# Kernel optimization log

Hardware: AMD Instinct MI355X
Metric: run time of the kernel (lower is better)

The kernel has to match this reference:

```python
import jax, jax.numpy as jnp
import numpy as np

B, C, H, W = 8, 256, 64, 64
K = 64  # tfam_channels

def _conv3x3(x, w, b):
    # x: [B,C,H,W], w: [O,I,3,3]
    y = jax.lax.conv_general_dilated(x, w, window_strides=(1, 1), padding='SAME',
                                     dimension_numbers=('NCHW', 'OIHW', 'NCHW'))
    return y + b[None, :, None, None]

def setup_inputs() -> dict:
    key = jax.random.key(0)
    ks = jax.random.split(key, 5)
    s1 = 1.0 / np.sqrt(C)
    s3 = 1.0 / np.sqrt(C * 9)
    return {
        'x': jax.random.normal(ks[0], (B, C, H, W), jnp.float32),
        'top_w': jax.random.normal(ks[1], (K, C), jnp.float32) * s1,
        'top_b': jnp.zeros((K,), jnp.float32),
        'center_w': jax.random.normal(ks[2], (K, C), jnp.float32) * s1,
        'center_b': jnp.zeros((K,), jnp.float32),
        'bottom_w': jax.random.normal(ks[3], (C, C, 3, 3), jnp.float32) * s3,
        'bottom_b': jnp.zeros((C,), jnp.float32),
        'out_w': jax.random.normal(ks[4], (C, C, 3, 3), jnp.float32) * s3,
        'out_b': jnp.zeros((C,), jnp.float32),
    }

def reference(x, top_w, top_b, center_w, center_b, bottom_w, bottom_b, out_w, out_b):
    b, c, h, w = x.shape
    hw = h * w
    # 1x1 convs as channel contractions
    x_top = jnp.einsum('bchw,kc->bkhw', x, top_w) + top_b[None, :, None, None]
    x_center = jnp.einsum('bchw,kc->bkhw', x, center_w) + center_b[None, :, None, None]
    x_bottom = _conv3x3(x, bottom_w, bottom_b)

    x_top = x_top.reshape(b, -1, hw)                     # [B,K,HW]
    x_center = x_center.reshape(b, -1, hw)               # [B,K,HW]
    x_bot = x_bottom.reshape(b, c, hw).transpose(0, 2, 1)  # [B,HW,C]

    sp_map = jnp.einsum('bkn,bkm->bnm', x_center, x_top)  # [B,HW,HW]
    # global softmax over the entire flattened map per batch element
    sp_map = jax.nn.softmax(sp_map.reshape(b, -1), axis=1).reshape(b, hw, hw)
    sp_map = jnp.einsum('bnm,bmc->bnc', sp_map, x_bot)    # [B,HW,C]
    # faithful raw reshape (as in the torch code: no transpose)
    sp_map = sp_map.reshape(b, c, h, w)
    y = x + sp_map
    return _conv3x3(y, out_w, out_b)
```

## Files before the change

kernel.cpp:

```cpp
#include <hip/hip_runtime.h>

using bf16x8 = __attribute__((ext_vector_type(8))) short;
using f16x8  = __attribute__((ext_vector_type(8))) _Float16;
using f32x4  = __attribute__((ext_vector_type(4))) float;

#define DEVI static __device__ __forceinline__

DEVI unsigned short f2bf(float f){
  unsigned u = __builtin_bit_cast(unsigned, f);
  u += 0x7fffu + ((u >> 16) & 1u);
  return (unsigned short)(u >> 16);
}
DEVI float bf2f(unsigned short h){
  unsigned u = ((unsigned)h) << 16;
  return __builtin_bit_cast(float, u);
}
DEVI unsigned short f2h(float f){
  _Float16 h = (_Float16)f;
  return __builtin_bit_cast(unsigned short, h);
}
DEVI f32x4 zf4(){ f32x4 z; z[0]=0.f; z[1]=0.f; z[2]=0.f; z[3]=0.f; return z; }
DEVI unsigned cvtpk(float lo, float hi){
  unsigned r;
  asm("v_cvt_pk_bf16_f32 %0, %1, %2" : "=v"(r) : "v"(lo), "v"(hi));
  return r;
}

__global__ __launch_bounds__(256) void k_prep(
    const float* __restrict__ top_w, const float* __restrict__ cen_w,
    const float* __restrict__ bot_w, const float* __restrict__ out_w,
    float* __restrict__ wTt, float* __restrict__ wTc,
    unsigned short* __restrict__ apb, unsigned short* __restrict__ apo){
  int i = blockIdx.x * 256 + threadIdx.x;
  if (i < 64 * 256){
    int c = i >> 6, k = i & 63;
    wTt[i] = top_w[k * 256 + c];
    wTc[i] = cen_w[k * 256 + c];
  }
  if (i < 9 * 256 * 256){
    int tau = i >> 16, oc = i & 65535;
    apb[i] = f2bf(bot_w[oc * 9 + tau]);
    apo[i] = f2bf(out_w[oc * 9 + tau]);
  }
}

__global__ __launch_bounds__(256) void k_topcenter(
    const float* __restrict__ x,
    const float* __restrict__ wTt, const float* __restrict__ wTc,
    const float* __restrict__ top_b, const float* __restrict__ cen_b,
    unsigned short* __restrict__ tT16, unsigned short* __restrict__ cT16){
  __shared__ float xs[16][256];
  int bid = blockIdx.x;
  int b = bid & 7, z = (bid >> 3) & 1, nt = (bid >> 4) & 15, kq = bid >> 8;
  int t = threadIdx.x;
  int n = nt * 256 + t;
  int k0 = kq * 16;
  const float* wT   = z ? wTc : wTt;
  const float* bias = z ? cen_b : top_b;
  unsigned short* o16 = z ? cT16 : tT16;
  const float scale = z ? 1.0f : 1.4426950408889634f;
  const float* xb = x + ((size_t)b << 20);

  float acc[16];
  #pragma unroll
  for (int k = 0; k < 16; k++) acc[k] = 0.f;

  for (int cc = 0; cc < 256; cc += 16){
    __syncthreads();
    #pragma unroll
    for (int r = 0; r < 16; r++)
      xs[r][t] = xb[((size_t)(cc + r) << 12) + nt * 256 + t];
    __syncthreads();
    #pragma unroll
    for (int r = 0; r < 16; r++){
      float xv = xs[r][t];
      const float* wr = wT + (cc + r) * 64 + k0;
      #pragma unroll
      for (int k = 0; k < 16; k++) acc[k] = fmaf(wr[k], xv, acc[k]);
    }
  }
  size_t base = (((size_t)b << 12) + n) * 64 + k0;
  #pragma unroll
  for (int k8 = 0; k8 < 16; k8 += 8){
    bf16x8 v8;
    #pragma unroll
    for (int j = 0; j < 8; j++)
      v8[j] = (short)f2h((acc[k8 + j] + bias[k0 + k8 + j]) * scale);
    *(bf16x8*)(o16 + base + k8) = v8;
  }
}

__global__ __launch_bounds__(256) void k_transx(
    const float* __restrict__ x, unsigned short* __restrict__ ocl){
  __shared__ float tile[32][33];
  int b = blockIdx.z, ct = blockIdx.y, pt = blockIdx.x;
  int tx = threadIdx.x & 31, ty = threadIdx.x >> 5;
  size_t bo = (size_t)b << 20;
  int c0 = ct * 32, p0 = pt * 32;
  #pragma unroll
  for (int q = 0; q < 4; q++){
    int c = c0 + ty + q * 8;
    tile[ty + q * 8][tx] = x[bo + ((size_t)c << 12) + p0 + tx];
  }
  __syncthreads();
  #pragma unroll
  for (int q = 0; q < 4; q++){
    int p = p0 + ty + q * 8;
    ocl[bo + ((size_t)p << 8) + c0 + tx] = f2bf(tile[tx][ty + q * 8]);
  }
}

__global__ __launch_bounds__(256) void k_transy(
    const float* __restrict__ x, const unsigned short* __restrict__ U0,
    const unsigned short* __restrict__ U1, const float* __restrict__ Z,
    unsigned short* __restrict__ ocl){
  __shared__ float tile[32][33];
  int b = blockIdx.z, ct = blockIdx.y, pt = blockIdx.x;
  int tx = threadIdx.x & 31, ty = threadIdx.x >> 5;
  size_t bo = (size_t)b << 20;
  int c0 = ct * 32, p0 = pt * 32;
  float invZ = 1.0f / Z[b];
  #pragma unroll
  for (int q = 0; q < 4; q++){
    int c = c0 + ty + q * 8;
    size_t idx = bo + ((size_t)c << 12) + p0 + tx;
    float u = bf2f(U0[idx]);
    if (U1) u += bf2f(U1[idx]);
    tile[ty + q * 8][tx] = fmaf(u, invZ, x[idx]);
  }
  __syncthreads();
  #pragma unroll
  for (int q = 0; q < 4; q++){
    int p = p0 + ty + q * 8;
    ocl[bo + ((size_t)p << 8) + c0 + tx] = f2bf(tile[tx][ty + q * 8]);
  }
}

template<int OUTF32>
__global__ __launch_bounds__(256, 4) void k_conv3(
    const unsigned short* __restrict__ incl,
    const unsigned short* __restrict__ ap,
    const float* __restrict__ bias, void* __restrict__ outp){
  __shared__ unsigned short Xs[3][64][72];
  int bid = blockIdx.x;
  int b = bid & 7, h = (bid >> 3) & 63, oh = bid >> 9;
  int t = threadIdx.x, wv = t >> 6, l = t & 63, lr = l & 15, g = l >> 4;
  int o0 = oh * 128 + wv * 32;
  const unsigned short* inb = incl + ((size_t)b << 20);

  f32x4 acc[2][4];
  #pragma unroll
  for (int a = 0; a < 2; a++)
    #pragma unroll
    for (int c = 0; c < 4; c++) acc[a][c] = zf4();

  int sw = t >> 2, sco = (t & 3) * 16;
  const bf16x8 zero8 = {0,0,0,0,0,0,0,0};

  bf16x8 st[3][2];
  #pragma unroll
  for (int r = 0; r < 3; r++){
    int h2 = h + r - 1;
    bool v = (unsigned)h2 < 64u;
    #pragma unroll
    for (int u = 0; u < 2; u++)
      st[r][u] = v ? *(const bf16x8*)(inb + (((size_t)(h2 * 64 + sw)) << 8)
                                      + sco + u * 8)
                   : zero8;
  }

  for (int cc = 0; cc < 256; cc += 64){
    __syncthreads();
    #pragma unroll
    for (int r = 0; r < 3; r++)
      #pragma unroll
      for (int u = 0; u < 2; u++)
        *(bf16x8*)(&Xs[r][sw][sco + u * 8]) = st[r][u];
    __syncthreads();
    if (cc < 192){
      #pragma unroll
      for (int r = 0; r < 3; r++){
        int h2 = h + r - 1;
        bool v = (unsigned)h2 < 64u;
        #pragma unroll
        for (int u = 0; u < 2; u++)
          st[r][u] = v ? *(const bf16x8*)(inb + (((size_t)(h2 * 64 + sw)) << 8)
                                          + cc + 64 + sco + u * 8)
                       : zero8;
      }
    }
    #pragma unroll
    for (int tau = 0; tau < 9; tau++){
      int dy = tau / 3 - 1, dx = tau % 3 - 1;
      #pragma unroll
      for (int kf = 0; kf < 2; kf++){
        bf16x8 af[2];
        #pragma unroll
        for (int of = 0; of < 2; of++)
          af[of] = *(const bf16x8*)(ap + ((size_t)tau << 16)
                     + ((o0 + of * 16 + lr) << 8) + cc + kf * 32 + 8 * g);
        bf16x8 bv[4];
        #pragma unroll
        for (int pf = 0; pf < 4; pf++){
          int wsrc = pf * 16 + lr + dx;
          bv[pf] = ((unsigned)wsrc < 64u)
                 ? *(const bf16x8*)(&Xs[dy + 1][wsrc][kf * 32 + 8 * g])
                 : zero8;
        }
        #pragma unroll
        for (int of = 0; of < 2; of++)
          #pragma unroll
          for (int pf = 0; pf < 4; pf++){
            if (OUTF32)
              acc[of][pf] = __builtin_amdgcn_mfma_f32_16x16x32_bf16(af[of], bv[pf], acc[of][pf], 0, 0, 0);
            else
              acc[of][pf] = __builtin_amdgcn_mfma_f32_16x16x32_bf16(bv[pf], af[of], acc[of][pf], 0, 0, 0);
          }
      }
    }
  }
  if (OUTF32){
    #pragma unroll
    for (int of = 0; of < 2; of++){
      int ob = o0 + of * 16 + 4 * g;
      #pragma unroll
      for (int pf = 0; pf < 4; pf++){
        int p = h * 64 + pf * 16 + lr;
        #pragma unroll
        for (int i = 0; i < 4; i++){
          int o = ob + i;
          ((float*)outp)[((size_t)b << 20) + ((size_t)o << 12) + p]
              = acc[of][pf][i] + bias[o];
        }
      }
    }
  } else {
    unsigned short* xbt = (unsigned short*)outp;
    #pragma unroll
    for (int of = 0; of < 2; of++){
      int o = o0 + of * 16 + lr;
      float bo_ = bias[o];
      #pragma unroll
      for (int pf = 0; pf < 4; pf++){
        int mc = h * 8 + pf * 2 + (g >> 1);
        unsigned lo = cvtpk(acc[of][pf][0] + bo_, acc[of][pf][1] + bo_);
        unsigned hi = cvtpk(acc[of][pf][2] + bo_, acc[of][pf][3] + bo_);
        unsigned* dst = (unsigned*)(xbt
            + ((((size_t)b * 512 + mc) * 256 + o) * 8 + 4 * (g & 1)));
        dst[0] = lo;
        dst[1] = hi;
      }
    }
  }
}

__global__ __launch_bounds__(256, 2) void k_pv(
    const unsigned short* __restrict__ tT16, const unsigned short* __restrict__ cT16,
    const unsigned short* __restrict__ xbt,
    unsigned short* __restrict__ U0, unsigned short* __restrict__ U1,
    float* __restrict__ rsum, int nsteps){
  __shared__ unsigned short Xl[2][4][256][8];
  __shared__ unsigned short Pl[2][4][128][8];
  int bid = blockIdx.x;
  int b = bid & 7, nt = (bid >> 3) & 31, mh = bid >> 8;
  int t = threadIdx.x, wv = t >> 6, l = t & 63, lr = l & 15, g = l >> 4;
  int n0 = nt * 128;
  unsigned short* Ub = mh ? U1 : U0;

  f16x8 ch[2][4];
  #pragma unroll
  for (int kf = 0; kf < 2; kf++)
    #pragma unroll
    for (int nf = 0; nf < 4; nf++)
      ch[kf][nf] = *(const f16x8*)(cT16
          + (((size_t)b << 12) + n0 + (wv >> 1) * 64 + nf * 16 + lr) * 64
          + kf * 32 + 8 * g);

  f32x4 acc[8][4];
  #pragma unroll
  for (int a = 0; a < 8; a++)
    #pragma unroll
    for (int c = 0; c < 4; c++) acc[a][c] = zf4();
  float racc = 0.f;

  const unsigned short* tb = tT16
      + (((size_t)b << 12) + (size_t)mh * 2048 + (wv & 1) * 16 + lr) * 64 + 8 * g;

  const unsigned short* gsrc = xbt
      + (((size_t)b * 512 + (size_t)mh * 256) * 256 + wv * 64 + l) * 8;

  int mt2 = (wv & 1) * 2 + (g >> 1);
  f16x8 a0 = *(const f16x8*)(tb);
  f16x8 a1 = *(const f16x8*)(tb + 32);

  {
    #pragma unroll
    for (int j = 0; j < 4; j++)
      __builtin_amdgcn_global_load_lds(
          (const __attribute__((address_space(1))) void*)(gsrc + (size_t)j * 2048),
          (__attribute__((address_space(3))) void*)(&Xl[0][j][wv * 64][0]),
          16, 0, 0);
    f32x4 sa[4];
    #pragma unroll
    for (int nf = 0; nf < 4; nf++) sa[nf] = zf4();
    #pragma unroll
    for (int nf = 0; nf < 4; nf++)
      sa[nf] = __builtin_amdgcn_mfma_f32_16x16x32_f16(a0, ch[0][nf], sa[nf], 0, 0, 0);
    #pragma unroll
    for (int nf = 0; nf < 4; nf++)
      sa[nf] = __builtin_amdgcn_mfma_f32_16x16x32_f16(a1, ch[1][nf], sa[nf], 0, 0, 0);
    a0 = *(const f16x8*)(tb + 2048);
    a1 = *(const f16x8*)(tb + 2048 + 32);
    #pragma unroll
    for (int nf = 0; nf < 4; nf++){
      float e0 = __builtin_amdgcn_exp2f(sa[nf][0]);
      float e1 = __builtin_amdgcn_exp2f(sa[nf][1]);
      float e2 = __builtin_amdgcn_exp2f(sa[nf][2]);
      float e3 = __builtin_amdgcn_exp2f(sa[nf][3]);
      racc += (e0 + e1) + (e2 + e3);
      int n = (wv >> 1) * 64 + nf * 16 + lr;
      unsigned* pp = (unsigned*)(&Pl[0][mt2][n][(g & 1) * 4]);
      pp[0] = cvtpk(e0, e1);
      pp[1] = cvtpk(e2, e3);
    }
    __syncthreads();
  }

  for (int ms = 0; ms < nsteps; ms++){
    int cur = ms & 1, nxt = cur ^ 1;
    bool more = (ms + 1 < nsteps);
    f32x4 sa[4];
    #pragma unroll
    for (int nf = 0; nf < 4; nf++) sa[nf] = zf4();
    if (more){
      #pragma unroll
      for (int j = 0; j < 4; j++)
        __builtin_amdgcn_global_load_lds(
            (const __attribute__((address_space(1))) void*)(gsrc + (size_t)((ms + 1) * 4 + j) * 2048),
            (__attribute__((address_space(3))) void*)(&Xl[nxt][j][wv * 64][0]),
            16, 0, 0);
      #pragma unroll
      for (int nf = 0; nf < 4; nf++)
        sa[nf] = __builtin_amdgcn_mfma_f32_16x16x32_f16(a0, ch[0][nf], sa[nf], 0, 0, 0);
      #pragma unroll
      for (int nf = 0; nf < 4; nf++)
        sa[nf] = __builtin_amdgcn_mfma_f32_16x16x32_f16(a1, ch[1][nf], sa[nf], 0, 0, 0);
      if (ms + 2 < nsteps){
        a0 = *(const f16x8*)(tb + (size_t)(ms + 2) * 2048);
        a1 = *(const f16x8*)(tb + (size_t)(ms + 2) * 2048 + 32);
      }
    }
    {
      bf16x8 pa[8];
      #pragma unroll
      for (int nf = 0; nf < 8; nf++)
        pa[nf] = *(const bf16x8*)(&Pl[cur][g][nf * 16 + lr][0]);
      #pragma unroll
      for (int cf = 0; cf < 4; cf++){
        bf16x8 bx = *(const bf16x8*)(&Xl[cur][g][wv * 64 + cf * 16 + lr][0]);
        #pragma unroll
        for (int nf = 0; nf < 8; nf++)
          acc[nf][cf] = __builtin_amdgcn_mfma_f32_16x16x32_bf16(pa[nf], bx, acc[nf][cf], 0, 0, 0);
      }
    }
    if (more){
      #pragma unroll
      for (int nf = 0; nf < 4; nf++){
        float e0 = __builtin_amdgcn_exp2f(sa[nf][0]);
        float e1 = __builtin_amdgcn_exp2f(sa[nf][1]);
        float e2 = __builtin_amdgcn_exp2f(sa[nf][2]);
        float e3 = __builtin_amdgcn_exp2f(sa[nf][3]);
        racc += (e0 + e1) + (e2 + e3);
        int n = (wv >> 1) * 64 + nf * 16 + lr;
        unsigned* pp = (unsigned*)(&Pl[nxt][mt2][n][(g & 1) * 4]);
        pp[0] = cvtpk(e0, e1);
        pp[1] = cvtpk(e2, e3);
      }
    }
    __syncthreads();
  }

  #pragma unroll
  for (int nf = 0; nf < 8; nf++)
    #pragma unroll
    for (int cf = 0; cf < 4; cf++)
      #pragma unroll
      for (int i = 0; i < 4; i++){
        int n = n0 + nf * 16 + 4 * g + i;
        int c = wv * 64 + cf * 16 + lr;
        __builtin_nontemporal_store(f2bf(acc[nf][cf][i]),
            &Ub[((size_t)b << 20) + ((size_t)n << 8) + c]);
      }
  racc += __shfl_xor(racc, 1);
  racc += __shfl_xor(racc, 2);
  racc += __shfl_xor(racc, 4);
  racc += __shfl_xor(racc, 8);
  racc += __shfl_xor(racc, 16);
  racc += __shfl_xor(racc, 32);
  if (l == 0) rsum[(size_t)bid * 4 + wv] = racc;
}

__global__ __launch_bounds__(256) void k_rsum(const float* __restrict__ r,
                                              float* __restrict__ Z, int total){
  __shared__ float red[256];
  int b = blockIdx.x, t = threadIdx.x;
  float s = 0.f;
  for (int s2 = t; s2 < total; s2 += 256)
    s += r[(size_t)(b + 8 * (s2 >> 2)) * 4 + (s2 & 3)];
  red[t] = s;
  __syncthreads();
  for (int o = 128; o > 0; o >>= 1){
    if (t < o) red[t] += red[t + o];
    __syncthreads();
  }
  if (t == 0) Z[b] = red[0];
}

extern "C" void kernel_launch(void* const* d_in, const int* in_sizes, int n_in,
                              void* d_out, int out_size, void* d_ws, size_t ws_size,
                              hipStream_t stream) {
  const float* x     = (const float*)d_in[0];
  const float* top_w = (const float*)d_in[1];
  const float* top_b = (const float*)d_in[2];
  const float* cen_w = (const float*)d_in[3];
  const float* cen_b = (const float*)d_in[4];
  const float* bot_w = (const float*)d_in[5];
  const float* bot_b = (const float*)d_in[6];
  const float* out_w = (const float*)d_in[7];
  const float* out_b = (const float*)d_in[8];
  float* out = (float*)d_out;

  constexpr size_t MB = 1ull << 20;
  int msplit = (ws_size >= 80 * MB) ? 2 : 1;

  char* p = (char*)d_ws;
  unsigned short* U0 = (unsigned short*)p;     p += 16 * MB;
  unsigned short* U1 = nullptr;
  if (msplit == 2){ U1 = (unsigned short*)p;   p += 16 * MB; }
  unsigned short* tT16 = (unsigned short*)p;   p += 4 * MB;
  unsigned short* cT16 = (unsigned short*)p;   p += 4 * MB;
  unsigned short* xbt  = (unsigned short*)p;   p += 16 * MB;
  unsigned short* xcl  = (unsigned short*)p;   p += 16 * MB;
  float* wTt = (float*)p;                      p += 65536;
  float* wTc = (float*)p;                      p += 65536;
  unsigned short* apb = (unsigned short*)p;    p += 1179648;
  unsigned short* apo = (unsigned short*)p;    p += 1179648;
  float* r = (float*)p;                        p += 65536;
  float* Z = (float*)p;

  int grid_pv = 8 * 32 * msplit;
  int nsteps  = (4096 / msplit) / 32;
  int slots   = (grid_pv / 8) * 4;

  k_prep<<<2304, 256, 0, stream>>>(top_w, cen_w, bot_w, out_w, wTt, wTc, apb, apo);
  k_topcenter<<<dim3(1024), 256, 0, stream>>>(x, wTt, wTc, top_b, cen_b,
                                              tT16, cT16);
  k_transx<<<dim3(128, 8, 8), 256, 0, stream>>>(x, xcl);
  k_conv3<0><<<dim3(1024), 256, 0, stream>>>(xcl, apb, bot_b, (void*)xbt);
  k_pv<<<dim3(grid_pv), 256, 0, stream>>>(tT16, cT16, xbt, U0,
                                          msplit == 2 ? U1 : U0, r, nsteps);
  k_rsum<<<8, 256, 0, stream>>>(r, Z, slots);
  k_transy<<<dim3(128, 8, 8), 256, 0, stream>>>(x, U0, U1, Z, xcl);
  k_conv3<1><<<dim3(1024), 256, 0, stream>>>(xcl, apo, out_b, (void*)out);
}
```

Measured before the change: 304.4 us.

## Split PV reduction four ways over M and hand-schedule barriers in k_pv

Raises the split of the attention's M (key) dimension from two to four when the workspace is large enough. This quadruples the k_pv grid for better CU occupancy, and k_transy now sums four bf16 partial buffers. It also replaces __syncthreads with explicit lgkmcnt waits, s_barrier and sched_barrier fences, and drops the barrier after the final step, to cut redundant waits. The cost is extra partial-buffer traffic and workspace, more bf16 rounding of partials, and activation depends on ws_size reaching 107 MB.

```diff
diff --git a/kernel.cpp b/kernel.cpp
--- a/kernel.cpp
+++ b/kernel.cpp
@@ -5,6 +5,7 @@
 using f32x4  = __attribute__((ext_vector_type(4))) float;
 
 #define DEVI static __device__ __forceinline__
+#define SCHEDB __builtin_amdgcn_sched_barrier(0)
 
 DEVI unsigned short f2bf(float f){
   unsigned u = __builtin_bit_cast(unsigned, f);
@@ -112,7 +113,8 @@
 
 __global__ __launch_bounds__(256) void k_transy(
     const float* __restrict__ x, const unsigned short* __restrict__ U0,
-    const unsigned short* __restrict__ U1, const float* __restrict__ Z,
+    const unsigned short* __restrict__ U1, const unsigned short* __restrict__ U2,
+    const unsigned short* __restrict__ U3, const float* __restrict__ Z,
     unsigned short* __restrict__ ocl){
   __shared__ float tile[32][33];
   int b = blockIdx.z, ct = blockIdx.y, pt = blockIdx.x;
@@ -126,6 +128,7 @@
     size_t idx = bo + ((size_t)c << 12) + p0 + tx;
     float u = bf2f(U0[idx]);
     if (U1) u += bf2f(U1[idx]);
+    if (U2) u += bf2f(U2[idx]) + bf2f(U3[idx]);
     tile[ty + q * 8][tx] = fmaf(u, invZ, x[idx]);
   }
   __syncthreads();
@@ -258,6 +261,7 @@
     const unsigned short* __restrict__ tT16, const unsigned short* __restrict__ cT16,
     const unsigned short* __restrict__ xbt,
     unsigned short* __restrict__ U0, unsigned short* __restrict__ U1,
+    unsigned short* __restrict__ U2, unsigned short* __restrict__ U3,
     float* __restrict__ rsum, int nsteps){
   __shared__ unsigned short Xl[2][4][256][8];
   __shared__ unsigned short Pl[2][4][128][8];
@@ -265,7 +269,8 @@
   int b = bid & 7, nt = (bid >> 3) & 31, mh = bid >> 8;
   int t = threadIdx.x, wv = t >> 6, l = t & 63, lr = l & 15, g = l >> 4;
   int n0 = nt * 128;
-  unsigned short* Ub = mh ? U1 : U0;
+  int mrows = nsteps * 32;
+  unsigned short* Ub = (mh == 0) ? U0 : (mh == 1) ? U1 : (mh == 2) ? U2 : U3;
 
   f16x8 ch[2][4];
   #pragma unroll
@@ -284,10 +289,10 @@
   float racc = 0.f;
 
   const unsigned short* tb = tT16
-      + (((size_t)b << 12) + (size_t)mh * 2048 + (wv & 1) * 16 + lr) * 64 + 8 * g;
+      + (((size_t)b << 12) + (size_t)mh * mrows + (wv & 1) * 16 + lr) * 64 + 8 * g;
 
   const unsigned short* gsrc = xbt
-      + (((size_t)b * 512 + (size_t)mh * 256) * 256 + wv * 64 + l) * 8;
+      + (((size_t)b * 512 + (size_t)mh * (mrows >> 3)) * 256 + wv * 64 + l) * 8;
 
   int mt2 = (wv & 1) * 2 + (g >> 1);
   f16x8 a0 = *(const f16x8*)(tb);
@@ -300,6 +305,7 @@
           (const __attribute__((address_space(1))) void*)(gsrc + (size_t)j * 2048),
           (__attribute__((address_space(3))) void*)(&Xl[0][j][wv * 64][0]),
           16, 0, 0);
+    SCHEDB;
     f32x4 sa[4];
     #pragma unroll
     for (int nf = 0; nf < 4; nf++) sa[nf] = zf4();
@@ -323,7 +329,10 @@
       pp[0] = cvtpk(e0, e1);
       pp[1] = cvtpk(e2, e3);
     }
-    __syncthreads();
+    asm volatile("s_waitcnt lgkmcnt(0)" ::: "memory");
+    SCHEDB;
+    __builtin_amdgcn_s_barrier();
+    SCHEDB;
   }
 
   for (int ms = 0; ms < nsteps; ms++){
@@ -339,6 +348,7 @@
             (const __attribute__((address_space(1))) void*)(gsrc + (size_t)((ms + 1) * 4 + j) * 2048),
             (__attribute__((address_space(3))) void*)(&Xl[nxt][j][wv * 64][0]),
             16, 0, 0);
+      SCHEDB;
       #pragma unroll
       for (int nf = 0; nf < 4; nf++)
         sa[nf] = __builtin_amdgcn_mfma_f32_16x16x32_f16(a0, ch[0][nf], sa[nf], 0, 0, 0);
@@ -349,6 +359,9 @@
         a0 = *(const f16x8*)(tb + (size_t)(ms + 2) * 2048);
         a1 = *(const f16x8*)(tb + (size_t)(ms + 2) * 2048 + 32);
       }
+    } else {
+      asm volatile("s_waitcnt vmcnt(0)" ::: "memory");
+      SCHEDB;
     }
     {
       bf16x8 pa[8];
@@ -376,8 +389,11 @@
         pp[0] = cvtpk(e0, e1);
         pp[1] = cvtpk(e2, e3);
       }
-    }
-    __syncthreads();
+      asm volatile("s_waitcnt lgkmcnt(0)" ::: "memory");
+      SCHEDB;
+      __builtin_amdgcn_s_barrier();
+      SCHEDB;
+    }
   }
 
   #pragma unroll
@@ -431,12 +447,18 @@
   float* out = (float*)d_out;
 
   constexpr size_t MB = 1ull << 20;
-  int msplit = (ws_size >= 80 * MB) ? 2 : 1;
+  int msplit = (ws_size >= 107 * MB) ? 4 : (ws_size >= 75 * MB ? 2 : 1);
 
   char* p = (char*)d_ws;
   unsigned short* U0 = (unsigned short*)p;     p += 16 * MB;
   unsigned short* U1 = nullptr;
-  if (msplit == 2){ U1 = (unsigned short*)p;   p += 16 * MB; }
+  unsigned short* U2 = nullptr;
+  unsigned short* U3 = nullptr;
+  if (msplit >= 2){ U1 = (unsigned short*)p;   p += 16 * MB; }
+  if (msplit == 4){
+    U2 = (unsigned short*)p;                   p += 16 * MB;
+    U3 = (unsigned short*)p;                   p += 16 * MB;
+  }
   unsigned short* tT16 = (unsigned short*)p;   p += 4 * MB;
   unsigned short* cT16 = (unsigned short*)p;   p += 4 * MB;
   unsigned short* xbt  = (unsigned short*)p;   p += 16 * MB;
@@ -458,8 +480,11 @@
   k_transx<<<dim3(128, 8, 8), 256, 0, stream>>>(x, xcl);
   k_conv3<0><<<dim3(1024), 256, 0, stream>>>(xcl, apb, bot_b, (void*)xbt);
   k_pv<<<dim3(grid_pv), 256, 0, stream>>>(tT16, cT16, xbt, U0,
-                                          msplit == 2 ? U1 : U0, r, nsteps);
+                                          msplit >= 2 ? U1 : U0,
+                                          msplit == 4 ? U2 : nullptr,
+                                          msplit == 4 ? U3 : nullptr,
+                                          r, nsteps);
   k_rsum<<<8, 256, 0, stream>>>(r, Z, slots);
-  k_transy<<<dim3(128, 8, 8), 256, 0, stream>>>(x, U0, U1, Z, xcl);
+  k_transy<<<dim3(128, 8, 8), 256, 0, stream>>>(x, U0, U1, U2, U3, Z, xcl);
   k_conv3<1><<<dim3(1024), 256, 0, stream>>>(xcl, apo, out_b, (void*)out);
 }
```

Measured after the change: 335.4 us. 1.1x slower.

## Compute two output rows per conv3x3 block to reuse weight fragments

Applied to the files above, without the earlier changes.

The 3x3 conv kernel now handles two adjacent output rows per block. It stages four input rows in LDS and reuses each loaded weight fragment for both rows, which halves the global weight traffic per output and halves the grid size. The price is more accumulator registers, so launch bounds drop from 4 to 3 blocks per CU. Separately, k_pv now computes its split offsets from nsteps instead of hardcoded values, and the workspace threshold for choosing the two-way split is lowered so that path can activate with less workspace.

```diff
diff --git a/kernel.cpp b/kernel.cpp
--- a/kernel.cpp
+++ b/kernel.cpp
@@ -137,30 +137,33 @@
 }
 
 template<int OUTF32>
-__global__ __launch_bounds__(256, 4) void k_conv3(
+__global__ __launch_bounds__(256, 3) void k_conv3(
     const unsigned short* __restrict__ incl,
     const unsigned short* __restrict__ ap,
     const float* __restrict__ bias, void* __restrict__ outp){
-  __shared__ unsigned short Xs[3][64][72];
+  __shared__ unsigned short Xs[4][64][72];
   int bid = blockIdx.x;
-  int b = bid & 7, h = (bid >> 3) & 63, oh = bid >> 9;
+  int b = bid & 7, hp = (bid >> 3) & 31, oh = bid >> 8;
+  int h0 = hp * 2;
   int t = threadIdx.x, wv = t >> 6, l = t & 63, lr = l & 15, g = l >> 4;
   int o0 = oh * 128 + wv * 32;
   const unsigned short* inb = incl + ((size_t)b << 20);
 
-  f32x4 acc[2][4];
-  #pragma unroll
-  for (int a = 0; a < 2; a++)
-    #pragma unroll
-    for (int c = 0; c < 4; c++) acc[a][c] = zf4();
+  f32x4 acc[2][2][4];
+  #pragma unroll
+  for (int rr = 0; rr < 2; rr++)
+    #pragma unroll
+    for (int a = 0; a < 2; a++)
+      #pragma unroll
+      for (int c = 0; c < 4; c++) acc[rr][a][c] = zf4();
 
   int sw = t >> 2, sco = (t & 3) * 16;
   const bf16x8 zero8 = {0,0,0,0,0,0,0,0};
 
-  bf16x8 st[3][2];
-  #pragma unroll
-  for (int r = 0; r < 3; r++){
-    int h2 = h + r - 1;
+  bf16x8 st[4][2];
+  #pragma unroll
+  for (int r = 0; r < 4; r++){
+    int h2 = h0 - 1 + r;
     bool v = (unsigned)h2 < 64u;
     #pragma unroll
     for (int u = 0; u < 2; u++)
@@ -172,15 +175,15 @@
   for (int cc = 0; cc < 256; cc += 64){
     __syncthreads();
     #pragma unroll
-    for (int r = 0; r < 3; r++)
+    for (int r = 0; r < 4; r++)
       #pragma unroll
       for (int u = 0; u < 2; u++)
         *(bf16x8*)(&Xs[r][sw][sco + u * 8]) = st[r][u];
     __syncthreads();
     if (cc < 192){
       #pragma unroll
-      for (int r = 0; r < 3; r++){
-        int h2 = h + r - 1;
+      for (int r = 0; r < 4; r++){
+        int h2 = h0 - 1 + r;
         bool v = (unsigned)h2 < 64u;
         #pragma unroll
         for (int u = 0; u < 2; u++)
@@ -199,58 +202,65 @@
         for (int of = 0; of < 2; of++)
           af[of] = *(const bf16x8*)(ap + ((size_t)tau << 16)
                      + ((o0 + of * 16 + lr) << 8) + cc + kf * 32 + 8 * g);
-        bf16x8 bv[4];
-        #pragma unroll
-        for (int pf = 0; pf < 4; pf++){
-          int wsrc = pf * 16 + lr + dx;
-          bv[pf] = ((unsigned)wsrc < 64u)
-                 ? *(const bf16x8*)(&Xs[dy + 1][wsrc][kf * 32 + 8 * g])
-                 : zero8;
-        }
-        #pragma unroll
-        for (int of = 0; of < 2; of++)
+        #pragma unroll
+        for (int rr = 0; rr < 2; rr++){
+          bf16x8 bv[4];
           #pragma unroll
           for (int pf = 0; pf < 4; pf++){
-            if (OUTF32)
-              acc[of][pf] = __builtin_amdgcn_mfma_f32_16x16x32_bf16(af[of], bv[pf], acc[of][pf], 0, 0, 0);
-            else
-              acc[of][pf] = __builtin_amdgcn_mfma_f32_16x16x32_bf16(bv[pf], af[of], acc[of][pf], 0, 0, 0);
+            int wsrc = pf * 16 + lr + dx;
+            bv[pf] = ((unsigned)wsrc < 64u)
+                   ? *(const bf16x8*)(&Xs[1 + rr + dy][wsrc][kf * 32 + 8 * g])
+                   : zero8;
           }
+          #pragma unroll
+          for (int of = 0; of < 2; of++)
+            #pragma unroll
+            for (int pf = 0; pf < 4; pf++){
+              if (OUTF32)
+                acc[rr][of][pf] = __builtin_amdgcn_mfma_f32_16x16x32_bf16(af[of], bv[pf], acc[rr][of][pf], 0, 0, 0);
+              else
+                acc[rr][of][pf] = __builtin_amdgcn_mfma_f32_16x16x32_bf16(bv[pf], af[of], acc[rr][of][pf], 0, 0, 0);
+            }
+        }
       }
     }
   }
   if (OUTF32){
     #pragma unroll
-    for (int of = 0; of < 2; of++){
-      int ob = o0 + of * 16 + 4 * g;
-      #pragma unroll
-      for (int pf = 0; pf < 4; pf++){
-        int p = h * 64 + pf * 16 + lr;
-        #pragma unroll
-        for (int i = 0; i < 4; i++){
-          int o = ob + i;
-          ((float*)outp)[((size_t)b << 20) + ((size_t)o << 12) + p]
-              = acc[of][pf][i] + bias[o];
+    for (int rr = 0; rr < 2; rr++)
+      #pragma unroll
+      for (int of = 0; of < 2; of++){
+        int ob = o0 + of * 16 + 4 * g;
+        #pragma unroll
+        for (int pf = 0; pf < 4; pf++){
+          int p = (h0 + rr) * 64 + pf * 16 + lr;
+          #pragma unroll
+          for (int i = 0; i < 4; i++){
+            int o = ob + i;
+            ((float*)outp)[((size_t)b << 20) + ((size_t)o << 12) + p]
+                = acc[rr][of][pf][i] + bias[o];
+          }
         }
       }
-    }
   } else {
     unsigned short* xbt = (unsigned short*)outp;
     #pragma unroll
-    for (int of = 0; of < 2; of++){
-      int o = o0 + of * 16 + lr;
-      float bo_ = bias[o];
-      #pragma unroll
-      for (int pf = 0; pf < 4; pf++){
-        int mc = h * 8 + pf * 2 + (g >> 1);
-        unsigned lo = cvtpk(acc[of][pf][0] + bo_, acc[of][pf][1] + bo_);
-        unsigned hi = cvtpk(acc[of][pf][2] + bo_, acc[of][pf][3] + bo_);
-        unsigned* dst = (unsigned*)(xbt
-            + ((((size_t)b * 512 + mc) * 256 + o) * 8 + 4 * (g & 1)));
-        dst[0] = lo;
-        dst[1] = hi;
-      }
-    }
+    for (int rr = 0; rr < 2; rr++)
+      #pragma unroll
+      for (int of = 0; of < 2; of++){
+        int o = o0 + of * 16 + lr;
+        float bo_ = bias[o];
+        #pragma unroll
+        for (int pf = 0; pf < 4; pf++){
+          int mc = (h0 + rr) * 8 + pf * 2 + (g >> 1);
+          unsigned lo = cvtpk(acc[rr][of][pf][0] + bo_, acc[rr][of][pf][1] + bo_);
+          unsigned hi = cvtpk(acc[rr][of][pf][2] + bo_, acc[rr][of][pf][3] + bo_);
+          unsigned* dst = (unsigned*)(xbt
+              + ((((size_t)b * 512 + mc) * 256 + o) * 8 + 4 * (g & 1)));
+          dst[0] = lo;
+          dst[1] = hi;
+        }
+      }
   }
 }
 
@@ -265,6 +275,7 @@
   int b = bid & 7, nt = (bid >> 3) & 31, mh = bid >> 8;
   int t = threadIdx.x, wv = t >> 6, l = t & 63, lr = l & 15, g = l >> 4;
   int n0 = nt * 128;
+  int mrows = nsteps * 32;
   unsigned short* Ub = mh ? U1 : U0;
 
   f16x8 ch[2][4];
@@ -284,10 +295,10 @@
   float racc = 0.f;
 
   const unsigned short* tb = tT16
-      + (((size_t)b << 12) + (size_t)mh * 2048 + (wv & 1) * 16 + lr) * 64 + 8 * g;
+      + (((size_t)b << 12) + (size_t)mh * mrows + (wv & 1) * 16 + lr) * 64 + 8 * g;
 
   const unsigned short* gsrc = xbt
-      + (((size_t)b * 512 + (size_t)mh * 256) * 256 + wv * 64 + l) * 8;
+      + (((size_t)b * 512 + (size_t)mh * (mrows >> 3)) * 256 + wv * 64 + l) * 8;
 
   int mt2 = (wv & 1) * 2 + (g >> 1);
   f16x8 a0 = *(const f16x8*)(tb);
@@ -431,7 +442,7 @@
   float* out = (float*)d_out;
 
   constexpr size_t MB = 1ull << 20;
-  int msplit = (ws_size >= 80 * MB) ? 2 : 1;
+  int msplit = (ws_size >= 75 * MB) ? 2 : 1;
 
   char* p = (char*)d_ws;
   unsigned short* U0 = (unsigned short*)p;     p += 16 * MB;
@@ -456,10 +467,10 @@
   k_topcenter<<<dim3(1024), 256, 0, stream>>>(x, wTt, wTc, top_b, cen_b,
                                               tT16, cT16);
   k_transx<<<dim3(128, 8, 8), 256, 0, stream>>>(x, xcl);
-  k_conv3<0><<<dim3(1024), 256, 0, stream>>>(xcl, apb, bot_b, (void*)xbt);
+  k_conv3<0><<<dim3(512), 256, 0, stream>>>(xcl, apb, bot_b, (void*)xbt);
   k_pv<<<dim3(grid_pv), 256, 0, stream>>>(tT16, cT16, xbt, U0,
                                           msplit == 2 ? U1 : U0, r, nsteps);
   k_rsum<<<8, 256, 0, stream>>>(r, Z, slots);
   k_transy<<<dim3(128, 8, 8), 256, 0, stream>>>(x, U0, U1, Z, xcl);
-  k_conv3<1><<<dim3(1024), 256, 0, stream>>>(xcl, apo, out_b, (void*)out);
-}
+  k_conv3<1><<<dim3(512), 256, 0, stream>>>(xcl, apo, out_b, (void*)out);
+}
```

New measurement: 375.1 us. 1.23x slower.
